# Kernel optimization log

Measured on AMD Instinct MI355X. Metric: run time of the kernel, lower is better.

## Reference

```python
import jax, jax.numpy as jnp
import numpy as np
from jax import lax

B, CIN, COUT, H, W = 4, 256, 256, 64, 64
KH = KW = 3
STRIDE = PAD = DIL = 1
GROUPS = 1
K = KH * KW
HO = (H + 2 * PAD - DIL * (KH - 1) - 1) // STRIDE + 1
WO = (W + 2 * PAD - DIL * (KW - 1) - 1) // STRIDE + 1
DN = ('NCHW', 'OIHW', 'NCHW')


def _sep_conv(x, dw, pw):
    # Separable2d: depthwise kxk conv (stride/pad/dilation) then pointwise 1x1.
    y = lax.conv_general_dilated(x, dw, (STRIDE, STRIDE), [(PAD, PAD), (PAD, PAD)],
                                 rhs_dilation=(DIL, DIL), feature_group_count=x.shape[1],
                                 dimension_numbers=DN)
    return lax.conv_general_dilated(y, pw, (1, 1), 'VALID', dimension_numbers=DN)


def _deform_conv2d(x, offset, mask, weight, bias):
    Bb, Cin, Hh, Ww = x.shape
    O = weight.shape[0]
    G = offset.shape[1] // (2 * K)  # offset groups
    offs = offset.reshape(Bb, G, K, 2, HO, WO)
    dy, dx = offs[:, :, :, 0], offs[:, :, :, 1]  # [B,G,K,Ho,Wo]
    ki, kj = jnp.meshgrid(jnp.arange(KH), jnp.arange(KW), indexing='ij')
    base_y = (-PAD + ki.reshape(K, 1) * DIL + jnp.arange(HO)[None, :] * STRIDE).astype(x.dtype)  # [K,Ho]
    base_x = (-PAD + kj.reshape(K, 1) * DIL + jnp.arange(WO)[None, :] * STRIDE).astype(x.dtype)  # [K,Wo]
    py = base_y[None, None, :, :, None] + dy  # [B,G,K,Ho,Wo]
    px = base_x[None, None, :, None, :] + dx

    xg = x.reshape(Bb, G, Cin // G, Hh, Ww)

    def bilinear(img, py, px):
        # img [C,H,W], py/px [K,Ho,Wo]; zero-padding outside bounds.
        y0 = jnp.floor(py)
        x0 = jnp.floor(px)
        out = jnp.zeros((img.shape[0],) + py.shape, img.dtype)
        for a, (iy, wy) in enumerate((((y0), (y0 + 1 - py)), ((y0 + 1), (py - y0)))):
            for b, (ix, wx) in enumerate((((x0), (x0 + 1 - px)), ((x0 + 1), (px - x0)))):
                valid = (iy >= 0) & (iy < Hh) & (ix >= 0) & (ix < Ww)
                iyc = jnp.clip(iy, 0, Hh - 1).astype(jnp.int32)
                ixc = jnp.clip(ix, 0, Ww - 1).astype(jnp.int32)
                v = img[:, iyc, ixc]  # [C,K,Ho,Wo]
                out = out + v * (wy * wx * valid)[None]
        return out

    sampled = jax.vmap(jax.vmap(bilinear))(xg, py, px)  # [B,G,C/G,K,Ho,Wo]
    m = mask.reshape(Bb, G, K, HO, WO)
    sampled = sampled * m[:, :, None]

    cols = sampled.reshape(Bb, Cin, K, HO, WO).reshape(Bb, GROUPS, Cin // GROUPS, K, HO, WO)
    wr = weight.reshape(GROUPS, O // GROUPS, Cin // GROUPS, K)
    out = jnp.einsum('bgckhw,gock->bgohw', cols, wr).reshape(Bb, O, HO, WO)
    return out + bias[None, :, None, None]


def setup_inputs() -> dict:
    key = jax.random.key(0)
    ks = jax.random.split(key, 7)
    x = jax.random.normal(ks[0], (B, CIN, H, W), jnp.float32)
    weight = jax.random.normal(ks[1], (COUT, CIN // GROUPS, KH, KW), jnp.float32) / np.sqrt(CIN * K)
    bias = jax.random.normal(ks[2], (COUT,), jnp.float32) * 0.01
    off_dw = jax.random.normal(ks[3], (CIN, 1, KH, KW), jnp.float32) * 0.01
    off_pw = jax.random.normal(ks[4], (2 * K * GROUPS, CIN, 1, 1), jnp.float32) * 0.01
    mask_dw = jax.random.normal(ks[5], (CIN, 1, KH, KW), jnp.float32) * 0.01
    mask_pw = jax.random.normal(ks[6], (K * GROUPS, CIN, 1, 1), jnp.float32) * 0.01
    return dict(x=x, weight=weight, bias=bias, off_dw=off_dw, off_pw=off_pw,
                mask_dw=mask_dw, mask_pw=mask_pw)


def reference(x, weight, bias, off_dw, off_pw, mask_dw, mask_pw):
    offset = _sep_conv(x, off_dw, off_pw)                       # [B,2*K,Ho,Wo]
    mask = jax.nn.sigmoid(_sep_conv(x, mask_dw, mask_pw)) * 2.0  # MaskSigmoid(scale=2)
    return _deform_conv2d(x, offset, mask, weight, bias)
```

## Files before the change

kernel.cpp:

```cpp
#include <hip/hip_runtime.h>

#define CIN   256
#define COUT  256
#define HH    64
#define WW    64
#define KD    2304
#define NPIX  16384
#define SPLIT 16
#define CPS   (CIN / SPLIT)

typedef __attribute__((ext_vector_type(8))) short  short8v;
typedef __attribute__((ext_vector_type(4))) float  float4v;
typedef __attribute__((ext_vector_type(2))) unsigned int uint2v;
typedef _Float16 h2 __attribute__((ext_vector_type(2)));
typedef _Float16 h8 __attribute__((ext_vector_type(8)));
typedef unsigned int u32;
typedef unsigned short u16;

__device__ __forceinline__ h2 as_h2(u32 v) { union { u32 u; h2 h; } x; x.u = v; return x.h; }
__device__ __forceinline__ u32 as_u32(h2 h) { union { u32 u; h2 h; } x; x.h = h; return x.u; }
__device__ __forceinline__ u16 f2h_bits(float f) { _Float16 h = (_Float16)f; return *(u16*)&h; }

__device__ __forceinline__ void gload_lds16(const void* g, void* l) {
  __builtin_amdgcn_global_load_lds((const __attribute__((address_space(1))) u32*)g,
                                   (__attribute__((address_space(3))) u32*)l, 16, 0, 0);
}

__global__ __launch_bounds__(256) void offmask_part_kernel(
    const float* __restrict__ x,
    const float* __restrict__ off_dw, const float* __restrict__ off_pw,
    const float* __restrict__ mask_dw, const float* __restrict__ mask_pw,
    float* __restrict__ part)
{
  int m = blockIdx.x * 256 + threadIdx.x;
  int s = blockIdx.y;
  int b = m >> 12, pix = m & 4095;
  int ho = pix >> 6, wo = pix & 63;
  const float* xb = x + (size_t)b * CIN * 4096;

  float acc[27];
#pragma unroll
  for (int j = 0; j < 27; ++j) acc[j] = 0.f;

  int c0 = s * CPS;
  for (int ci = 0; ci < CPS; ++ci) {
    int c = c0 + ci;
    const float* xc = xb + (size_t)c * 4096;
    float d_off = 0.f, d_msk = 0.f;
#pragma unroll
    for (int t = 0; t < 9; ++t) {
      int gy = ho + t / 3 - 1, gx = wo + t % 3 - 1;
      bool ok = (gy >= 0) & (gy < HH) & (gx >= 0) & (gx < WW);
      float v = ok ? xc[gy * 64 + gx] : 0.f;
      d_off += v * off_dw[c * 9 + t];
      d_msk += v * mask_dw[c * 9 + t];
    }
#pragma unroll
    for (int j = 0; j < 18; ++j) acc[j] += d_off * off_pw[j * 256 + c];
#pragma unroll
    for (int j = 0; j < 9; ++j) acc[18 + j] += d_msk * mask_pw[j * 256 + c];
  }
  float* pp = part + ((size_t)s * NPIX + m) * 32;
#pragma unroll
  for (int j = 0; j < 27; ++j) pp[j] = acc[j];
}

__global__ __launch_bounds__(256) void offmask_reduce_kernel(
    const float* __restrict__ part, float* __restrict__ rec)
{
  int i = blockIdx.x * 256 + threadIdx.x;
  int m = i >> 5, j = i & 31;
  if (j >= 27) { rec[i] = 0.f; return; }
  float sum = 0.f;
#pragma unroll
  for (int s = 0; s < SPLIT; ++s) sum += part[((size_t)s * NPIX + m) * 32 + j];
  rec[i] = (j < 18) ? sum : 2.f / (1.f + __expf(-sum));
}

__global__ __launch_bounds__(256) void wconv_kernel(const float* __restrict__ w,
                                                    u16* __restrict__ wb)
{
  int i = blockIdx.x * 256 + threadIdx.x;
  int co = i / KD, rem = i - co * KD;
  int c = rem / 9, kk = rem - c * 9;
  wb[co * KD + kk * 256 + c] = f2h_bits(w[i]);
}

__global__ __launch_bounds__(256) void xpose_kernel(const float* __restrict__ x,
                                                    u16* __restrict__ xt)
{
  __shared__ float t[64][65];
  int ptile = blockIdx.x;
  int ctile = blockIdx.y;
  int b     = blockIdx.z;
  int tid = threadIdx.x;
  const float* xb = x + (size_t)b * CIN * 4096 + (size_t)ctile * 64 * 4096 + ptile * 64;
#pragma unroll
  for (int i = 0; i < 16; ++i) {
    int c = i * 4 + (tid >> 6), p = tid & 63;
    t[c][p] = xb[(size_t)c * 4096 + p];
  }
  __syncthreads();
  u16* xo = xt + ((size_t)b * 4096 + ptile * 64) * 256 + ctile * 64;
#pragma unroll
  for (int i = 0; i < 16; ++i) {
    int p = i * 4 + (tid >> 6), c = tid & 63;
    xo[(size_t)p * 256 + c] = f2h_bits(t[c][p]);
  }
}

__global__ __launch_bounds__(512) void gemm_fused_kernel(
    const u16* __restrict__ A,
    const u16* __restrict__ xt,
    const float* __restrict__ rec,
    const float* __restrict__ bias,
    float* __restrict__ out,
    float* __restrict__ tmp)
{
  __shared__ __align__(16) u16 lA[2][256 * 32];
  __shared__ __align__(16) u16 lB[2][64 * 32];
  const int tid = threadIdx.x;
  const int bid = blockIdx.x;
  const int h   = bid & 3;
  const int ptile = bid >> 2;
  const int m0  = ptile * 64;
  const int b_img = ptile >> 6;
  const int cbase = h * 64;
  const int wave = tid >> 6, lane = tid & 63;
  const int wm = wave >> 1, wn = wave & 1;
  const int rl = lane & 15, kq = lane >> 4;
  const int sA = (kq ^ (rl & 3) ^ ((rl >> 2) & 3)) * 8;

  const int rA  = tid >> 2;
  const int koA = ((tid & 3) ^ (rA & 3) ^ ((rA >> 2) & 3)) * 8;
  const u16* aRow0 = A + (size_t)rA * KD + koA;
  const u16* aRow1 = A + (size_t)(rA + 128) * KD + koA;

  const int spx = tid >> 3;
  const int sc4 = (tid & 7) * 4;
  const int m_px = m0 + spx;
  const int ho = (m_px & 4095) >> 6, wo = m_px & 63;
  const float* rp = rec + (size_t)m_px * 32;
  const u16* xb = xt + (size_t)b_img * 4096 * 256;
  const int wAddr = spx * 32 +
                    ((((tid >> 1) & 3) ^ ((spx & 3) ^ ((spx >> 2) & 3))) * 8) +
                    (tid & 1) * 4;

  u32 cOff[4];
  h2  wh[4];

#define KCOL(t_) (((t_) >> 1) * 256 + cbase + ((t_) & 1) * 32)

#define CALC_CORNERS(kk_) do {                                             \
    float dy = rp[(kk_) * 2], dx = rp[(kk_) * 2 + 1], msk = rp[18 + (kk_)];\
    float py  = (float)(ho - 1 + ((kk_) / 3)) + dy;                        \
    float pxf = (float)(wo - 1 + ((kk_) % 3)) + dx;                        \
    float fy = floorf(py), fx = floorf(pxf);                               \
    int y0 = (int)fy, x0 = (int)fx;                                        \
    float wy1 = py - fy, wy0 = 1.f - wy1;                                  \
    float wx1 = pxf - fx, wx0 = 1.f - wx1;                                 \
    _Pragma("unroll")                                                      \
    for (int cr = 0; cr < 4; ++cr) {                                       \
      int iy = y0 + (cr >> 1), ix = x0 + (cr & 1);                         \
      bool valid = (iy >= 0) & (iy < HH) & (ix >= 0) & (ix < WW);          \
      int iyc = min(max(iy, 0), HH - 1), ixc = min(max(ix, 0), WW - 1);    \
      cOff[cr] = (u32)(iyc * 64 + ixc) * 256;                              \
      float wy = (cr >> 1) ? wy1 : wy0;                                    \
      float wx = (cr & 1) ? wx1 : wx0;                                     \
      float wf = valid ? (wy * wx * msk) : 0.f;                            \
      _Float16 hw = (_Float16)wf;                                          \
      wh[cr] = (h2){hw, hw};                                               \
    }                                                                      \
  } while (0)

#define STAGE_A(t, bufi) do {                                              \
    int k0_ = KCOL(t);                                                     \
    gload_lds16(aRow0 + k0_, lA[bufi] + tid * 8);                          \
    gload_lds16(aRow1 + k0_, lA[bufi] + (tid + 512) * 8);                  \
  } while (0)

#define BLEND_WRITE(bufi, v0_, v1_, v2_, v3_) do {                         \
    h2 a01 = wh[0] * as_h2((v0_)[0]) + wh[1] * as_h2((v1_)[0]);            \
    a01   += wh[2] * as_h2((v2_)[0]) + wh[3] * as_h2((v3_)[0]);            \
    h2 a23 = wh[0] * as_h2((v0_)[1]) + wh[1] * as_h2((v1_)[1]);            \
    a23   += wh[2] * as_h2((v2_)[1]) + wh[3] * as_h2((v3_)[1]);            \
    uint2v wv; wv[0] = as_u32(a01); wv[1] = as_u32(a23);                   \
    *(uint2v*)&lB[bufi][wAddr] = wv;                                       \
  } while (0)

  float4v acc[4][2];
#pragma unroll
  for (int m = 0; m < 4; ++m)
#pragma unroll
    for (int n = 0; n < 2; ++n) acc[m][n] = float4v{0.f, 0.f, 0.f, 0.f};

  {
    CALC_CORNERS(0);
    int c0n = cbase + sc4;
    uint2v v0 = *(const uint2v*)(xb + cOff[0] + c0n);
    uint2v v1 = *(const uint2v*)(xb + cOff[1] + c0n);
    uint2v v2 = *(const uint2v*)(xb + cOff[2] + c0n);
    uint2v v3 = *(const uint2v*)(xb + cOff[3] + c0n);
    BLEND_WRITE(0, v0, v1, v2, v3);
    STAGE_A(0, 0);
  }
  __syncthreads();

#pragma unroll 2
  for (int ks = 0; ks < 18; ++ks) {
    const int cur = ks & 1;
    uint2v v0, v1, v2, v3;
    const bool have = (ks < 17);
    if (have) {
      STAGE_A(ks + 1, cur ^ 1);
      int ksn = ks + 1;
      if ((ksn & 1) == 0) CALC_CORNERS(ksn >> 1);
      int c0n = cbase + (ksn & 1) * 32 + sc4;
      v0 = *(const uint2v*)(xb + cOff[0] + c0n);
      v1 = *(const uint2v*)(xb + cOff[1] + c0n);
      v2 = *(const uint2v*)(xb + cOff[2] + c0n);
      v3 = *(const uint2v*)(xb + cOff[3] + c0n);
    }
    h8 af[4], bf[2];
#pragma unroll
    for (int m = 0; m < 4; ++m)
      af[m] = *(const h8*)&lA[cur][(wm * 64 + m * 16 + rl) * 32 + sA];
#pragma unroll
    for (int n = 0; n < 2; ++n)
      bf[n] = *(const h8*)&lB[cur][(wn * 32 + n * 16 + rl) * 32 + sA];
#pragma unroll
    for (int m = 0; m < 4; ++m)
#pragma unroll
      for (int n = 0; n < 2; ++n)
        acc[m][n] = __builtin_amdgcn_mfma_f32_16x16x32_f16(af[m], bf[n], acc[m][n], 0, 0, 0);
    if (have) BLEND_WRITE(cur ^ 1, v0, v1, v2, v3);
    __syncthreads();
  }
#undef STAGE_A
#undef CALC_CORNERS
#undef BLEND_WRITE
#undef KCOL

  const int p_base = (m0 & 4095) + wn * 32;
  float* db = (h ? (tmp + (size_t)(h - 1) * COUT * NPIX) : out) +
              (size_t)b_img * COUT * 4096;
#pragma unroll
  for (int m = 0; m < 4; ++m) {
#pragma unroll
    for (int j = 0; j < 4; ++j) {
      int co = wm * 64 + m * 16 + kq * 4 + j;
      float bv = h ? 0.f : bias[co];
#pragma unroll
      for (int n = 0; n < 2; ++n) {
        int pp = p_base + n * 16 + rl;
        db[(size_t)co * 4096 + pp] = acc[m][n][j] + bv;
      }
    }
  }
}

__global__ __launch_bounds__(256) void add_kernel(float* __restrict__ out,
                                                  const float* __restrict__ tmp)
{
  size_t i = ((size_t)blockIdx.x * 256 + threadIdx.x) * 4;
  float4v a  = *(const float4v*)(out + i);
  float4v b0 = *(const float4v*)(tmp + i);
  float4v b1 = *(const float4v*)(tmp + (size_t)COUT * NPIX + i);
  float4v b2 = *(const float4v*)(tmp + (size_t)2 * COUT * NPIX + i);
  a += b0 + b1 + b2;
  *(float4v*)(out + i) = a;
}

extern "C" void kernel_launch(void* const* d_in, const int* in_sizes, int n_in,
                              void* d_out, int out_size, void* d_ws, size_t ws_size,
                              hipStream_t stream) {
  const float* x       = (const float*)d_in[0];
  const float* weight  = (const float*)d_in[1];
  const float* bias    = (const float*)d_in[2];
  const float* off_dw  = (const float*)d_in[3];
  const float* off_pw  = (const float*)d_in[4];
  const float* mask_dw = (const float*)d_in[5];
  const float* mask_pw = (const float*)d_in[6];

  if (ws_size < 61997056ull) return;
  float* rec  = (float*)d_ws;
  u16*   wb   = (u16*)((char*)d_ws + 2097152);
  u16*   xt   = (u16*)((char*)d_ws + 3276800);
  float* part = (float*)((char*)d_ws + 11665408);
  float* tmp  = part;
  float* out  = (float*)d_out;

  wconv_kernel<<<dim3(2304), dim3(256), 0, stream>>>(weight, wb);
  offmask_part_kernel<<<dim3(NPIX / 256, SPLIT), dim3(256), 0, stream>>>(
      x, off_dw, off_pw, mask_dw, mask_pw, part);
  offmask_reduce_kernel<<<dim3(NPIX * 32 / 256), dim3(256), 0, stream>>>(part, rec);
  xpose_kernel<<<dim3(64, 4, 4), dim3(256), 0, stream>>>(x, xt);
  gemm_fused_kernel<<<dim3(1024), dim3(512), 0, stream>>>(wb, xt, rec, bias, out, tmp);
  add_kernel<<<dim3(COUT * NPIX / 4 / 256), dim3(256), 0, stream>>>(out, tmp);
}
```

Measured before the change: 110.8 us.

## Halve split-K factor and triple-buffer weight tiles with manual waitcnt pipeline

The fused deformable-conv GEMM now splits the reduction across channels two ways instead of four, which halves the grid to 512 blocks and doubles the K steps per block to 36. This cuts the partial-sum scratch traffic and reduces the final add kernel to one extra buffer. Weight tiles are now triple-buffered in LDS and prefetched two steps ahead. The blocking __syncthreads is replaced with explicit vmcnt/lgkmcnt waits plus s_barrier. Fewer blocks lower parallelism on the many-CU GPU, and the launch bound is raised to request 4 waves per SIMD.

```diff
diff --git a/kernel.cpp b/kernel.cpp
--- a/kernel.cpp
+++ b/kernel.cpp
@@ -8,8 +8,8 @@
 #define NPIX  16384
 #define SPLIT 16
 #define CPS   (CIN / SPLIT)
-
-typedef __attribute__((ext_vector_type(8))) short  short8v;
+#define NSTEP 36
+
 typedef __attribute__((ext_vector_type(4))) float  float4v;
 typedef __attribute__((ext_vector_type(2))) unsigned int uint2v;
 typedef _Float16 h2 __attribute__((ext_vector_type(2)));
@@ -109,7 +109,7 @@
   }
 }
 
-__global__ __launch_bounds__(512) void gemm_fused_kernel(
+__global__ __launch_bounds__(512, 4) void gemm_fused_kernel(
     const u16* __restrict__ A,
     const u16* __restrict__ xt,
     const float* __restrict__ rec,
@@ -117,15 +117,15 @@
     float* __restrict__ out,
     float* __restrict__ tmp)
 {
-  __shared__ __align__(16) u16 lA[2][256 * 32];
+  __shared__ __align__(16) u16 lA[3][256 * 32];
   __shared__ __align__(16) u16 lB[2][64 * 32];
   const int tid = threadIdx.x;
   const int bid = blockIdx.x;
-  const int h   = bid & 3;
-  const int ptile = bid >> 2;
+  const int h   = bid & 1;
+  const int ptile = bid >> 1;
   const int m0  = ptile * 64;
   const int b_img = ptile >> 6;
-  const int cbase = h * 64;
+  const int cbase = h * 128;
   const int wave = tid >> 6, lane = tid & 63;
   const int wm = wave >> 1, wn = wave & 1;
   const int rl = lane & 15, kq = lane >> 4;
@@ -149,7 +149,7 @@
   u32 cOff[4];
   h2  wh[4];
 
-#define KCOL(t_) (((t_) >> 1) * 256 + cbase + ((t_) & 1) * 32)
+#define KCOL(t_) (((t_) >> 2) * 256 + cbase + ((t_) & 3) * 32)
 
 #define CALC_CORNERS(kk_) do {                                             \
     float dy = rp[(kk_) * 2], dx = rp[(kk_) * 2 + 1], msk = rp[18 + (kk_)];\
@@ -173,19 +173,19 @@
     }                                                                      \
   } while (0)
 
-#define STAGE_A(t, bufi) do {                                              \
-    int k0_ = KCOL(t);                                                     \
-    gload_lds16(aRow0 + k0_, lA[bufi] + tid * 8);                          \
-    gload_lds16(aRow1 + k0_, lA[bufi] + (tid + 512) * 8);                  \
+#define STAGE_A(k_, slot_) do {                                            \
+    int k0_ = KCOL(k_);                                                    \
+    gload_lds16(aRow0 + k0_, lA[slot_] + tid * 8);                         \
+    gload_lds16(aRow1 + k0_, lA[slot_] + (tid + 512) * 8);                 \
   } while (0)
 
-#define BLEND_WRITE(bufi, v0_, v1_, v2_, v3_) do {                         \
+#define BLEND_WRITE(bufi_, v0_, v1_, v2_, v3_) do {                        \
     h2 a01 = wh[0] * as_h2((v0_)[0]) + wh[1] * as_h2((v1_)[0]);            \
     a01   += wh[2] * as_h2((v2_)[0]) + wh[3] * as_h2((v3_)[0]);            \
     h2 a23 = wh[0] * as_h2((v0_)[1]) + wh[1] * as_h2((v1_)[1]);            \
     a23   += wh[2] * as_h2((v2_)[1]) + wh[3] * as_h2((v3_)[1]);            \
     uint2v wv; wv[0] = as_u32(a01); wv[1] = as_u32(a23);                   \
-    *(uint2v*)&lB[bufi][wAddr] = wv;                                       \
+    *(uint2v*)&lB[bufi_][wAddr] = wv;                                      \
   } while (0)
 
   float4v acc[4][2];
@@ -201,40 +201,44 @@
     uint2v v1 = *(const uint2v*)(xb + cOff[1] + c0n);
     uint2v v2 = *(const uint2v*)(xb + cOff[2] + c0n);
     uint2v v3 = *(const uint2v*)(xb + cOff[3] + c0n);
+    STAGE_A(0, 0);
+    STAGE_A(1, 1);
+    asm volatile("s_waitcnt vmcnt(2)" ::: "memory");
     BLEND_WRITE(0, v0, v1, v2, v3);
-    STAGE_A(0, 0);
-  }
-  __syncthreads();
-
-#pragma unroll 2
-  for (int ks = 0; ks < 18; ++ks) {
-    const int cur = ks & 1;
-    uint2v v0, v1, v2, v3;
-    const bool have = (ks < 17);
-    if (have) {
-      STAGE_A(ks + 1, cur ^ 1);
-      int ksn = ks + 1;
-      if ((ksn & 1) == 0) CALC_CORNERS(ksn >> 1);
-      int c0n = cbase + (ksn & 1) * 32 + sc4;
-      v0 = *(const uint2v*)(xb + cOff[0] + c0n);
-      v1 = *(const uint2v*)(xb + cOff[1] + c0n);
-      v2 = *(const uint2v*)(xb + cOff[2] + c0n);
-      v3 = *(const uint2v*)(xb + cOff[3] + c0n);
+    asm volatile("s_waitcnt lgkmcnt(0)" ::: "memory");
+    __builtin_amdgcn_s_barrier();
+  }
+
+  for (int it = 0; it < 6; ++it) {
+#pragma unroll
+    for (int u = 0; u < 6; ++u) {
+      const int t = it * 6 + u;
+      const int tn  = (t + 1 == NSTEP) ? 0 : t + 1;
+      const int tn2 = (t + 2 >= NSTEP) ? (t + 2 - NSTEP) : t + 2;
+      if ((tn & 3) == 0) CALC_CORNERS(tn >> 2);
+      int c0n = cbase + (tn & 3) * 32 + sc4;
+      uint2v v0 = *(const uint2v*)(xb + cOff[0] + c0n);
+      uint2v v1 = *(const uint2v*)(xb + cOff[1] + c0n);
+      uint2v v2 = *(const uint2v*)(xb + cOff[2] + c0n);
+      uint2v v3 = *(const uint2v*)(xb + cOff[3] + c0n);
+      STAGE_A(tn2, (u + 2) % 3);
+      h8 af[4], bf[2];
+#pragma unroll
+      for (int m = 0; m < 4; ++m)
+        af[m] = *(const h8*)&lA[u % 3][(wm * 64 + m * 16 + rl) * 32 + sA];
+#pragma unroll
+      for (int n = 0; n < 2; ++n)
+        bf[n] = *(const h8*)&lB[u & 1][(wn * 32 + n * 16 + rl) * 32 + sA];
+#pragma unroll
+      for (int m = 0; m < 4; ++m)
+#pragma unroll
+        for (int n = 0; n < 2; ++n)
+          acc[m][n] = __builtin_amdgcn_mfma_f32_16x16x32_f16(af[m], bf[n], acc[m][n], 0, 0, 0);
+      asm volatile("s_waitcnt vmcnt(2)" ::: "memory");
+      BLEND_WRITE((u + 1) & 1, v0, v1, v2, v3);
+      asm volatile("s_waitcnt lgkmcnt(0)" ::: "memory");
+      __builtin_amdgcn_s_barrier();
     }
-    h8 af[4], bf[2];
-#pragma unroll
-    for (int m = 0; m < 4; ++m)
-      af[m] = *(const h8*)&lA[cur][(wm * 64 + m * 16 + rl) * 32 + sA];
-#pragma unroll
-    for (int n = 0; n < 2; ++n)
-      bf[n] = *(const h8*)&lB[cur][(wn * 32 + n * 16 + rl) * 32 + sA];
-#pragma unroll
-    for (int m = 0; m < 4; ++m)
-#pragma unroll
-      for (int n = 0; n < 2; ++n)
-        acc[m][n] = __builtin_amdgcn_mfma_f32_16x16x32_f16(af[m], bf[n], acc[m][n], 0, 0, 0);
-    if (have) BLEND_WRITE(cur ^ 1, v0, v1, v2, v3);
-    __syncthreads();
   }
 #undef STAGE_A
 #undef CALC_CORNERS
@@ -242,8 +246,7 @@
 #undef KCOL
 
   const int p_base = (m0 & 4095) + wn * 32;
-  float* db = (h ? (tmp + (size_t)(h - 1) * COUT * NPIX) : out) +
-              (size_t)b_img * COUT * 4096;
+  float* db = (h ? tmp : out) + (size_t)b_img * COUT * 4096;
 #pragma unroll
   for (int m = 0; m < 4; ++m) {
 #pragma unroll
@@ -263,11 +266,9 @@
                                                   const float* __restrict__ tmp)
 {
   size_t i = ((size_t)blockIdx.x * 256 + threadIdx.x) * 4;
-  float4v a  = *(const float4v*)(out + i);
-  float4v b0 = *(const float4v*)(tmp + i);
-  float4v b1 = *(const float4v*)(tmp + (size_t)COUT * NPIX + i);
-  float4v b2 = *(const float4v*)(tmp + (size_t)2 * COUT * NPIX + i);
-  a += b0 + b1 + b2;
+  float4v a = *(const float4v*)(out + i);
+  float4v b = *(const float4v*)(tmp + i);
+  a += b;
   *(float4v*)(out + i) = a;
 }
 
@@ -282,7 +283,7 @@
   const float* mask_dw = (const float*)d_in[5];
   const float* mask_pw = (const float*)d_in[6];
 
-  if (ws_size < 61997056ull) return;
+  if (ws_size < 45219840ull) return;
   float* rec  = (float*)d_ws;
   u16*   wb   = (u16*)((char*)d_ws + 2097152);
   u16*   xt   = (u16*)((char*)d_ws + 3276800);
@@ -295,6 +296,6 @@
       x, off_dw, off_pw, mask_dw, mask_pw, part);
   offmask_reduce_kernel<<<dim3(NPIX * 32 / 256), dim3(256), 0, stream>>>(part, rec);
   xpose_kernel<<<dim3(64, 4, 4), dim3(256), 0, stream>>>(x, xt);
-  gemm_fused_kernel<<<dim3(1024), dim3(512), 0, stream>>>(wb, xt, rec, bias, out, tmp);
+  gemm_fused_kernel<<<dim3(512), dim3(512), 0, stream>>>(wb, xt, rec, bias, out, tmp);
   add_kernel<<<dim3(COUT * NPIX / 4 / 256), dim3(256), 0, stream>>>(out, tmp);
 }
```

Measured after the change: 107.1 us. 3.4% less time.
